# Kernel optimization log

Measured on AMD Instinct MI355X. Metric: run time of the kernel, lower is better.

## Reference

```python
import jax, jax.numpy as jnp
import numpy as np

KERNEL_SIZE = 4
STRIDE = 4


def setup_inputs() -> dict:
    key = jax.random.key(0)
    ks = jax.random.split(key, 5)
    b, l, d, hidden = 32, 8192, 256, 512
    x = jax.random.normal(ks[0], (b, l, d), dtype=jnp.float32)
    We = jax.random.normal(ks[1], (d, hidden), dtype=jnp.float32) * (1.0 / np.sqrt(d))
    be = jax.random.normal(ks[2], (hidden,), dtype=jnp.float32) * 0.01
    Wr = jax.random.normal(ks[3], (hidden, 1), dtype=jnp.float32) * (1.0 / np.sqrt(hidden))
    br = jax.random.normal(ks[4], (1,), dtype=jnp.float32) * 0.01
    return {"x": x, "We": We, "be": be, "Wr": Wr, "br": br}


def reference(x, We, be, Wr, br):
    b, l, d = x.shape
    steps = (l - KERNEL_SIZE) // STRIDE + 1
    # window gather: original loop slices x[:, i*stride : i*stride+stride, :]
    idx = jnp.arange(steps)[:, None] * STRIDE + jnp.arange(STRIDE)[None, :]  # (steps, stride)
    win = x[:, idx, :]  # (b, steps, stride, d)
    h = jnp.tanh(win @ We + be)                      # (b, steps, stride, hidden)
    logits = jnp.squeeze(h @ Wr, -1) + br            # (b, steps, stride)
    w = jax.nn.softmax(jax.nn.sigmoid(logits), axis=-1)
    out = jnp.einsum('bswd,bsw->bsd', win, w)        # softmax-weighted sum over window
    return out
```

## Files before the change

### kernel.cpp

```cpp
#include <hip/hip_runtime.h>
#include <hip/hip_bf16.h>

typedef __attribute__((ext_vector_type(8))) short bf16x8;
typedef __attribute__((ext_vector_type(4))) float f32x4;

#define D        256
#define NH       512
#define NT       32
#define KT       8
#define MT       4
#define ROWS_PER_BLOCK 64
#define ROWS_TOTAL (32*8192)

typedef __attribute__((address_space(1))) const void GV;
typedef __attribute__((address_space(3))) void LV;

__device__ __forceinline__ short f2bf(float f) {
    union { float f; unsigned u; } v; v.f = f;
    unsigned r = v.u + 0x7FFFu + ((v.u >> 16) & 1u);
    return (short)(r >> 16);
}
__device__ __forceinline__ float rcp_fast(float x) {
    return __builtin_amdgcn_rcpf(x);
}

__global__ void prepack_B(const float* __restrict__ We, const float* __restrict__ be,
                          const float* __restrict__ Wr,
                          short* __restrict__ Bh, float* __restrict__ bias2,
                          float* __restrict__ Ssum) {
    int i = blockIdx.x * 256 + threadIdx.x;
    int k = i >> 9;
    int n = i & 511;
    int nt = n >> 4, c = n & 15;
    int kt = k >> 5, g = (k >> 3) & 3, j = k & 7;
    int idx = (((nt * 8 + kt) * 64) + (g * 16 + c)) * 8 + j;
    Bh[idx] = f2bf(We[i]);
    if (i < 512) bias2[i] = 2.0f * be[i];
    if (i == 0) {
        float s = 0.0f;
        for (int t = 0; t < 512; ++t) s += Wr[t];
        Ssum[0] = s;
    }
}

__global__ __launch_bounds__(64, 2) void softpool_main(
    const float* __restrict__ x, const short* __restrict__ Bh,
    const float* __restrict__ bias2, const float* __restrict__ Wr,
    const float* __restrict__ br, const float* __restrict__ Ssum,
    float* __restrict__ out)
{
    const int lane = threadIdx.x;
    const int c = lane & 15;
    const int g = lane >> 4;
    const long row0 = (long)blockIdx.x * ROWS_PER_BLOCK;

    __shared__ short Bl[2][4096];

    const short* gB = Bh + lane * 8;

    #define STAGE(buf, ntv) {                                                  \
        const short* _g = gB + (long)(ntv) * 4096;                             \
        _Pragma("unroll")                                                      \
        for (int kk = 0; kk < 8; ++kk)                                         \
            __builtin_amdgcn_global_load_lds((GV*)(_g + kk * 512),             \
                (LV*)&Bl[buf][kk * 512], 16, 0, 0);                            \
    }

    STAGE(0, 0)

    bf16x8 a[MT][KT];
    #pragma unroll
    for (int m = 0; m < MT; ++m) {
        const float* xr = x + (row0 + m * 16 + c) * D + g * 8;
        #pragma unroll
        for (int kt = 0; kt < KT; ++kt) {
            float4 v0 = *(const float4*)(xr + kt * 32);
            float4 v1 = *(const float4*)(xr + kt * 32 + 4);
            bf16x8 t;
            t[0] = f2bf(v0.x); t[1] = f2bf(v0.y); t[2] = f2bf(v0.z); t[3] = f2bf(v0.w);
            t[4] = f2bf(v1.x); t[5] = f2bf(v1.y); t[6] = f2bf(v1.z); t[7] = f2bf(v1.w);
            a[m][kt] = t;
        }
    }

    float lps[MT][4];
    #pragma unroll
    for (int m = 0; m < MT; ++m)
        #pragma unroll
        for (int r = 0; r < 4; ++r) lps[m][r] = 0.0f;

    f32x4 accA[MT], accB[MT];

    #define MFMA_(buf, accv) {                                                 \
        _Pragma("unroll")                                                      \
        for (int m = 0; m < MT; ++m)                                           \
            _Pragma("unroll")                                                  \
            for (int r = 0; r < 4; ++r) accv[m][r] = 0.0f;                     \
        _Pragma("unroll")                                                      \
        for (int kt = 0; kt < KT; ++kt) {                                      \
            bf16x8 b = *(const bf16x8*)&Bl[buf][kt * 512 + lane * 8];          \
            _Pragma("unroll")                                                  \
            for (int m = 0; m < MT; ++m)                                       \
                accv[m] = __builtin_amdgcn_mfma_f32_16x16x32_bf16(             \
                             a[m][kt], b, accv[m], 0, 0, 0);                   \
        }                                                                      \
    }

    #define TANH_(accv, ntv) {                                                 \
        int n = (ntv) * 16 + c;                                                \
        float b2 = bias2[n];                                                   \
        float vr = Wr[n];                                                      \
        _Pragma("unroll")                                                      \
        for (int m = 0; m < MT; ++m)                                           \
            _Pragma("unroll")                                                  \
            for (int r = 0; r < 4; ++r) {                                      \
                float z = __builtin_fmaf(accv[m][r], 2.0f, b2);                \
                float e = __expf(z);                                           \
                float rr = rcp_fast(e + 1.0f);                                 \
                lps[m][r] = __builtin_fmaf(vr, rr, lps[m][r]);                 \
            }                                                                  \
    }

    #define WAITV0 asm volatile("s_waitcnt vmcnt(0)" ::: "memory");

    WAITV0

    STAGE(1, 1)
    MFMA_(0, accA)
    WAITV0
    for (int it = 0; it < 15; ++it) {
        const int ntB = 2 * it + 1;
        STAGE(0, ntB + 1)
        MFMA_(1, accB)
        TANH_(accA, ntB - 1)
        WAITV0
        const int ntA = 2 * it + 2;
        STAGE(1, ntA + 1)
        MFMA_(0, accA)
        TANH_(accB, ntA - 1)
        WAITV0
    }
    MFMA_(1, accB)
    TANH_(accA, 30)
    TANH_(accB, 31)

    const float brv = br[0];
    const float S = Ssum[0];
    #pragma unroll
    for (int m = 0; m < MT; ++m) {
        float l0 = lps[m][0], l1 = lps[m][1], l2 = lps[m][2], l3 = lps[m][3];
        #pragma unroll
        for (int off = 1; off < 16; off <<= 1) {
            l0 += __shfl_xor(l0, off, 64);
            l1 += __shfl_xor(l1, off, 64);
            l2 += __shfl_xor(l2, off, 64);
            l3 += __shfl_xor(l3, off, 64);
        }
        float g0 = S - 2.0f * l0 + brv;
        float g1 = S - 2.0f * l1 + brv;
        float g2 = S - 2.0f * l2 + brv;
        float g3 = S - 2.0f * l3 + brv;
        float s0 = rcp_fast(1.0f + __expf(-g0));
        float s1 = rcp_fast(1.0f + __expf(-g1));
        float s2 = rcp_fast(1.0f + __expf(-g2));
        float s3 = rcp_fast(1.0f + __expf(-g3));
        float e0 = __expf(s0), e1 = __expf(s1), e2 = __expf(s2), e3 = __expf(s3);
        float inv = rcp_fast(e0 + e1 + e2 + e3);
        float w0 = e0 * inv, w1 = e1 * inv, w2 = e2 * inv, w3 = e3 * inv;

        const long wrow = row0 + m * 16 + g * 4;
        const long W = wrow >> 2;
        const float* xw = x + wrow * D + c * 4;
        float* op = out + W * D + c * 4;
        #pragma unroll
        for (int q = 0; q < 4; ++q) {
            float4 r0 = *(const float4*)(xw + 0 * D + q * 64);
            float4 r1 = *(const float4*)(xw + 1 * D + q * 64);
            float4 r2 = *(const float4*)(xw + 2 * D + q * 64);
            float4 r3 = *(const float4*)(xw + 3 * D + q * 64);
            float4 oo;
            oo.x = w0 * r0.x + w1 * r1.x + w2 * r2.x + w3 * r3.x;
            oo.y = w0 * r0.y + w1 * r1.y + w2 * r2.y + w3 * r3.y;
            oo.z = w0 * r0.z + w1 * r1.z + w2 * r2.z + w3 * r3.z;
            oo.w = w0 * r0.w + w1 * r1.w + w2 * r2.w + w3 * r3.w;
            *(float4*)(op + q * 64) = oo;
        }
    }
}

extern "C" void kernel_launch(void* const* d_in, const int* in_sizes, int n_in,
                              void* d_out, int out_size, void* d_ws, size_t ws_size,
                              hipStream_t stream) {
    const float* x  = (const float*)d_in[0];
    const float* We = (const float*)d_in[1];
    const float* be = (const float*)d_in[2];
    const float* Wr = (const float*)d_in[3];
    const float* br = (const float*)d_in[4];
    float* out = (float*)d_out;

    char* ws = (char*)d_ws;
    short* Bh    = (short*)ws;
    float* bias2 = (float*)(ws + 262144);
    float* Ssum  = (float*)(ws + 262144 + 2048);

    prepack_B<<<NH * D / 256, 256, 0, stream>>>(We, be, Wr, Bh, bias2, Ssum);

    const int blocks = ROWS_TOTAL / ROWS_PER_BLOCK;
    softpool_main<<<blocks, 64, 0, stream>>>(x, Bh, bias2, Wr, br, Ssum, out);
}
```

Baseline: 161.8 us.

## Halve rows per block and stream B in half-tiles with partial vmcnt waits

Cuts the M tile from 64 to 32 rows per block and raises the launch bound to 4 waves, halving the LDS double buffer. B is now staged in half-tiles, and each wait uses s_waitcnt vmcnt(4) instead of a full drain, so one stage's loads stay in flight while the previous half is consumed by MFMA. The bias and Wr constants are packed into one float2 so each tanh step does a single load. The trade-off is that every block reloads the full B matrix, so the smaller tile doubles total B traffic through L2 in exchange for higher occupancy and better overlap.

```diff
diff --git a/kernel.cpp b/kernel.cpp
--- a/kernel.cpp
+++ b/kernel.cpp
@@ -8,8 +8,8 @@
 #define NH       512
 #define NT       32
 #define KT       8
-#define MT       4
-#define ROWS_PER_BLOCK 64
+#define MT       2
+#define ROWS_PER_BLOCK 32
 #define ROWS_TOTAL (32*8192)
 
 typedef __attribute__((address_space(1))) const void GV;
@@ -26,7 +26,7 @@
 
 __global__ void prepack_B(const float* __restrict__ We, const float* __restrict__ be,
                           const float* __restrict__ Wr,
-                          short* __restrict__ Bh, float* __restrict__ bias2,
+                          short* __restrict__ Bh, float2* __restrict__ bw,
                           float* __restrict__ Ssum) {
     int i = blockIdx.x * 256 + threadIdx.x;
     int k = i >> 9;
@@ -35,7 +35,7 @@
     int kt = k >> 5, g = (k >> 3) & 3, j = k & 7;
     int idx = (((nt * 8 + kt) * 64) + (g * 16 + c)) * 8 + j;
     Bh[idx] = f2bf(We[i]);
-    if (i < 512) bias2[i] = 2.0f * be[i];
+    if (i < 512) bw[i] = make_float2(2.0f * be[i], Wr[i]);
     if (i == 0) {
         float s = 0.0f;
         for (int t = 0; t < 512; ++t) s += Wr[t];
@@ -43,30 +43,31 @@
     }
 }
 
-__global__ __launch_bounds__(64, 2) void softpool_main(
+__global__ __launch_bounds__(64, 4) void softpool_main(
     const float* __restrict__ x, const short* __restrict__ Bh,
-    const float* __restrict__ bias2, const float* __restrict__ Wr,
-    const float* __restrict__ br, const float* __restrict__ Ssum,
-    float* __restrict__ out)
+    const float2* __restrict__ bw, const float* __restrict__ br,
+    const float* __restrict__ Ssum, float* __restrict__ out)
 {
     const int lane = threadIdx.x;
     const int c = lane & 15;
     const int g = lane >> 4;
     const long row0 = (long)blockIdx.x * ROWS_PER_BLOCK;
 
-    __shared__ short Bl[2][4096];
+    __shared__ short Bl[2][2048];
 
     const short* gB = Bh + lane * 8;
 
-    #define STAGE(buf, ntv) {                                                  \
-        const short* _g = gB + (long)(ntv) * 4096;                             \
-        _Pragma("unroll")                                                      \
-        for (int kk = 0; kk < 8; ++kk)                                         \
+    #define STAGE_HP(buf, hp) {                                                \
+        const short* _g = gB + (long)(hp) * 2048;                              \
+        _Pragma("unroll")                                                      \
+        for (int kk = 0; kk < 4; ++kk)                                         \
             __builtin_amdgcn_global_load_lds((GV*)(_g + kk * 512),             \
                 (LV*)&Bl[buf][kk * 512], 16, 0, 0);                            \
     }
 
-    STAGE(0, 0)
+    #define VM4 asm volatile("s_waitcnt vmcnt(4)" ::: "memory");
+
+    STAGE_HP(0, 0)
 
     bf16x8 a[MT][KT];
     #pragma unroll
@@ -91,57 +92,56 @@
 
     f32x4 accA[MT], accB[MT];
 
-    #define MFMA_(buf, accv) {                                                 \
+    #define HALF(buf, accv, ktb) {                                             \
+        _Pragma("unroll")                                                      \
+        for (int kk = 0; kk < 4; ++kk) {                                       \
+            bf16x8 b = *(const bf16x8*)&Bl[buf][kk * 512 + lane * 8];          \
+            _Pragma("unroll")                                                  \
+            for (int m = 0; m < MT; ++m)                                       \
+                accv[m] = __builtin_amdgcn_mfma_f32_16x16x32_bf16(             \
+                             a[m][(ktb) + kk], b, accv[m], 0, 0, 0);           \
+        }                                                                      \
+    }
+
+    #define ZERO(accv) {                                                       \
         _Pragma("unroll")                                                      \
         for (int m = 0; m < MT; ++m)                                           \
             _Pragma("unroll")                                                  \
             for (int r = 0; r < 4; ++r) accv[m][r] = 0.0f;                     \
-        _Pragma("unroll")                                                      \
-        for (int kt = 0; kt < KT; ++kt) {                                      \
-            bf16x8 b = *(const bf16x8*)&Bl[buf][kt * 512 + lane * 8];          \
-            _Pragma("unroll")                                                  \
-            for (int m = 0; m < MT; ++m)                                       \
-                accv[m] = __builtin_amdgcn_mfma_f32_16x16x32_bf16(             \
-                             a[m][kt], b, accv[m], 0, 0, 0);                   \
-        }                                                                      \
     }
 
     #define TANH_(accv, ntv) {                                                 \
-        int n = (ntv) * 16 + c;                                                \
-        float b2 = bias2[n];                                                   \
-        float vr = Wr[n];                                                      \
+        float2 bwv = bw[(ntv) * 16 + c];                                       \
         _Pragma("unroll")                                                      \
         for (int m = 0; m < MT; ++m)                                           \
             _Pragma("unroll")                                                  \
             for (int r = 0; r < 4; ++r) {                                      \
-                float z = __builtin_fmaf(accv[m][r], 2.0f, b2);                \
+                float z = __builtin_fmaf(accv[m][r], 2.0f, bwv.x);             \
                 float e = __expf(z);                                           \
                 float rr = rcp_fast(e + 1.0f);                                 \
-                lps[m][r] = __builtin_fmaf(vr, rr, lps[m][r]);                 \
+                lps[m][r] = __builtin_fmaf(bwv.y, rr, lps[m][r]);              \
             }                                                                  \
     }
 
-    #define WAITV0 asm volatile("s_waitcnt vmcnt(0)" ::: "memory");
-
-    WAITV0
-
-    STAGE(1, 1)
-    MFMA_(0, accA)
-    WAITV0
-    for (int it = 0; it < 15; ++it) {
-        const int ntB = 2 * it + 1;
-        STAGE(0, ntB + 1)
-        MFMA_(1, accB)
-        TANH_(accA, ntB - 1)
-        WAITV0
-        const int ntA = 2 * it + 2;
-        STAGE(1, ntA + 1)
-        MFMA_(0, accA)
-        TANH_(accB, ntA - 1)
-        WAITV0
-    }
-    MFMA_(1, accB)
-    TANH_(accA, 30)
+    for (int it = 0; it < 16; ++it) {
+        const int hp0 = 4 * it;
+        STAGE_HP(1, hp0 + 1)
+        VM4
+        ZERO(accA)
+        HALF(0, accA, 0)
+        STAGE_HP(0, hp0 + 2)
+        VM4
+        HALF(1, accA, 4)
+        if (it > 0) TANH_(accB, 2 * it - 1)
+        STAGE_HP(1, hp0 + 3)
+        VM4
+        ZERO(accB)
+        HALF(0, accB, 0)
+        STAGE_HP(0, (hp0 + 4) & 63)
+        VM4
+        HALF(1, accB, 4)
+        TANH_(accA, 2 * it)
+    }
     TANH_(accB, 31)
 
     const float brv = br[0];
@@ -199,12 +199,12 @@
     float* out = (float*)d_out;
 
     char* ws = (char*)d_ws;
-    short* Bh    = (short*)ws;
-    float* bias2 = (float*)(ws + 262144);
-    float* Ssum  = (float*)(ws + 262144 + 2048);
-
-    prepack_B<<<NH * D / 256, 256, 0, stream>>>(We, be, Wr, Bh, bias2, Ssum);
+    short*  Bh   = (short*)ws;
+    float2* bwp  = (float2*)(ws + 262144);
+    float*  Ssum = (float*)(ws + 262144 + 4096);
+
+    prepack_B<<<NH * D / 256, 256, 0, stream>>>(We, be, Wr, Bh, bwp, Ssum);
 
     const int blocks = ROWS_TOTAL / ROWS_PER_BLOCK;
-    softpool_main<<<blocks, 64, 0, stream>>>(x, Bh, bias2, Wr, br, Ssum, out);
-}
+    softpool_main<<<blocks, 64, 0, stream>>>(x, Bh, bwp, br, Ssum, out);
+}
```

Measured after the change: 173.8 us. +7.4%, slower.

## Replicate packed weights across workspace copies and stage bias/Wr pairs in LDS

Applied to the files above, without the earlier changes.

Prepack writes up to 8 copies of the bf16 weight fragments, and each block reads the copy selected by its block index. This spreads weight traffic across different addresses and cache channels, which should reduce contention on a single 256KB hot region. Bias and Wr are packed into float2 pairs, copied once into shared memory, and read from LDS in the tanh stage instead of from global memory. The cost is a larger prepack write and extra LDS use per block; the LDS copy has no barrier, but with a single-wave block this is likely safe.

```diff
diff --git a/kernel.cpp b/kernel.cpp
--- a/kernel.cpp
+++ b/kernel.cpp
@@ -11,6 +11,7 @@
 #define MT       4
 #define ROWS_PER_BLOCK 64
 #define ROWS_TOTAL (32*8192)
+#define BFRAG    131072
 
 typedef __attribute__((address_space(1))) const void GV;
 typedef __attribute__((address_space(3))) void LV;
@@ -26,16 +27,18 @@
 
 __global__ void prepack_B(const float* __restrict__ We, const float* __restrict__ be,
                           const float* __restrict__ Wr,
-                          short* __restrict__ Bh, float* __restrict__ bias2,
-                          float* __restrict__ Ssum) {
+                          short* __restrict__ Bh, float2* __restrict__ bw,
+                          float* __restrict__ Ssum, int ncopy) {
     int i = blockIdx.x * 256 + threadIdx.x;
     int k = i >> 9;
     int n = i & 511;
     int nt = n >> 4, c = n & 15;
     int kt = k >> 5, g = (k >> 3) & 3, j = k & 7;
     int idx = (((nt * 8 + kt) * 64) + (g * 16 + c)) * 8 + j;
-    Bh[idx] = f2bf(We[i]);
-    if (i < 512) bias2[i] = 2.0f * be[i];
+    short v = f2bf(We[i]);
+    for (int cp = 0; cp < ncopy; ++cp)
+        Bh[cp * BFRAG + idx] = v;
+    if (i < 512) bw[i] = make_float2(2.0f * be[i], Wr[i]);
     if (i == 0) {
         float s = 0.0f;
         for (int t = 0; t < 512; ++t) s += Wr[t];
@@ -45,9 +48,8 @@
 
 __global__ __launch_bounds__(64, 2) void softpool_main(
     const float* __restrict__ x, const short* __restrict__ Bh,
-    const float* __restrict__ bias2, const float* __restrict__ Wr,
-    const float* __restrict__ br, const float* __restrict__ Ssum,
-    float* __restrict__ out)
+    const float2* __restrict__ bwg, const float* __restrict__ br,
+    const float* __restrict__ Ssum, float* __restrict__ out, int cmask)
 {
     const int lane = threadIdx.x;
     const int c = lane & 15;
@@ -55,8 +57,9 @@
     const long row0 = (long)blockIdx.x * ROWS_PER_BLOCK;
 
     __shared__ short Bl[2][4096];
-
-    const short* gB = Bh + lane * 8;
+    __shared__ float2 bwl[512];
+
+    const short* gB = Bh + (long)(blockIdx.x & cmask) * BFRAG + lane * 8;
 
     #define STAGE(buf, ntv) {                                                  \
         const short* _g = gB + (long)(ntv) * 4096;                             \
@@ -66,7 +69,15 @@
                 (LV*)&Bl[buf][kk * 512], 16, 0, 0);                            \
     }
 
+    #define VM0 asm volatile("s_waitcnt vmcnt(0)" ::: "memory");
+
     STAGE(0, 0)
+
+    #pragma unroll
+    for (int i = 0; i < 4; ++i) {
+        float4 v = ((const float4*)bwg)[lane * 4 + i];
+        ((float4*)bwl)[lane * 4 + i] = v;
+    }
 
     bf16x8 a[MT][KT];
     #pragma unroll
@@ -107,38 +118,32 @@
     }
 
     #define TANH_(accv, ntv) {                                                 \
-        int n = (ntv) * 16 + c;                                                \
-        float b2 = bias2[n];                                                   \
-        float vr = Wr[n];                                                      \
+        float2 bwv = bwl[(ntv) * 16 + c];                                      \
         _Pragma("unroll")                                                      \
         for (int m = 0; m < MT; ++m)                                           \
             _Pragma("unroll")                                                  \
             for (int r = 0; r < 4; ++r) {                                      \
-                float z = __builtin_fmaf(accv[m][r], 2.0f, b2);                \
+                float z = __builtin_fmaf(accv[m][r], 2.0f, bwv.x);             \
                 float e = __expf(z);                                           \
                 float rr = rcp_fast(e + 1.0f);                                 \
-                lps[m][r] = __builtin_fmaf(vr, rr, lps[m][r]);                 \
+                lps[m][r] = __builtin_fmaf(bwv.y, rr, lps[m][r]);              \
             }                                                                  \
     }
 
-    #define WAITV0 asm volatile("s_waitcnt vmcnt(0)" ::: "memory");
-
-    WAITV0
-
+    VM0
     STAGE(1, 1)
     MFMA_(0, accA)
-    WAITV0
+    VM0
+
     for (int it = 0; it < 15; ++it) {
-        const int ntB = 2 * it + 1;
-        STAGE(0, ntB + 1)
+        STAGE(0, 2 * it + 2)
         MFMA_(1, accB)
-        TANH_(accA, ntB - 1)
-        WAITV0
-        const int ntA = 2 * it + 2;
-        STAGE(1, ntA + 1)
+        TANH_(accA, 2 * it)
+        VM0
+        STAGE(1, 2 * it + 3)
         MFMA_(0, accA)
-        TANH_(accB, ntA - 1)
-        WAITV0
+        TANH_(accB, 2 * it + 1)
+        VM0
     }
     MFMA_(1, accB)
     TANH_(accA, 30)
@@ -198,13 +203,15 @@
     const float* br = (const float*)d_in[4];
     float* out = (float*)d_out;
 
+    const int ncopy = (ws_size >= (size_t)8 * BFRAG * 2 + 8192) ? 8 : 1;
+
     char* ws = (char*)d_ws;
-    short* Bh    = (short*)ws;
-    float* bias2 = (float*)(ws + 262144);
-    float* Ssum  = (float*)(ws + 262144 + 2048);
-
-    prepack_B<<<NH * D / 256, 256, 0, stream>>>(We, be, Wr, Bh, bias2, Ssum);
+    short*  Bh   = (short*)ws;
+    float2* bwp  = (float2*)(ws + (size_t)ncopy * BFRAG * 2);
+    float*  Ssum = (float*)((char*)bwp + 4096);
+
+    prepack_B<<<BFRAG / 256, 256, 0, stream>>>(We, be, Wr, Bh, bwp, Ssum, ncopy);
 
     const int blocks = ROWS_TOTAL / ROWS_PER_BLOCK;
-    softpool_main<<<blocks, 64, 0, stream>>>(x, Bh, bias2, Wr, br, Ssum, out);
-}
+    softpool_main<<<blocks, 64, 0, stream>>>(x, Bh, bwp, br, Ssum, out, ncopy - 1);
+}
```

After: 163.1 us. Within noise of the previous version (+0.8%).
